# Optimization experiments

Hardware: AMD Instinct MI355X
Metric: run time of the kernel (lower is better)

Reference implementation:

```python
import jax, jax.numpy as jnp
import numpy as np

IN_CH, C_M, C_N = 512, 512, 128
B, H, W = 16, 56, 56


def setup_inputs() -> dict:
    key = jax.random.key(0)
    ks = jax.random.split(key, 7)
    s = 1.0 / np.sqrt(IN_CH)
    return {
        "x": jax.random.normal(ks[0], (B, IN_CH, H, W), dtype=jnp.float32),
        "wA": jax.random.uniform(ks[1], (C_M, IN_CH), jnp.float32, -s, s),
        "bA": jax.random.uniform(ks[2], (C_M,), jnp.float32, -s, s),
        "wB": jax.random.uniform(ks[3], (C_N, IN_CH), jnp.float32, -s, s),
        "bB": jax.random.uniform(ks[4], (C_N,), jnp.float32, -s, s),
        "wV": jax.random.uniform(ks[5], (C_N, IN_CH), jnp.float32, -s, s),
        "bV": jax.random.uniform(ks[6], (C_N,), jnp.float32, -s, s),
        "K": 1,
    }


def reference(x, wA, bA, wB, bB, wV, bV, K):
    b, c, h, w = x.shape
    c_m, c_n = wA.shape[0], wB.shape[0]
    batch = b // K
    hw = h * w
    N = K * hw
    # 1x1 convs == channel-wise matmuls
    A = jnp.einsum('bchw,mc->bmhw', x, wA) + bA[None, :, None, None]
    Bf = jnp.einsum('bchw,nc->bnhw', x, wB) + bB[None, :, None, None]
    Vf = jnp.einsum('bchw,nc->bnhw', x, wV) + bV[None, :, None, None]
    # (batch, c_m, K*h*w)
    tmpA = A.reshape(batch, K, c_m, hw).transpose(0, 2, 1, 3).reshape(batch, c_m, N)
    # softmax over the spatial dim N (torch Softmax() on 2D -> dim=1)
    tmpB = Bf.reshape(batch, K, c_n, hw).transpose(0, 2, 1, 3).reshape(batch, c_n, N)
    attB = jax.nn.softmax(tmpB, axis=-1).transpose(0, 2, 1)  # (batch, N, c_n)
    # softmax over channel dim c_n
    tmpV = Vf.reshape(batch, K, c_n, hw).transpose(0, 1, 3, 2).reshape(batch, N, c_n)
    attV = jax.nn.softmax(tmpV, axis=-1).transpose(0, 2, 1)  # (batch, c_n, N)
    G = jnp.matmul(tmpA, attB)   # (batch, c_m, c_n) global descriptors
    Z = jnp.matmul(G, attV)      # (batch, c_m, N) distribute
    Z = Z.reshape(batch, c_m, K, hw).transpose(0, 2, 1, 3).reshape(b, c_m, h, w)
    return Z
```

## Files before the change

kernel.cpp:

```cpp
#include <hip/hip_runtime.h>
#include <hip/hip_bf16.h>

#define BATCH 16
#define CIN   512
#define HW    3136
#define CM    512
#define CN    128

typedef short short8 __attribute__((ext_vector_type(8)));
typedef float f32x4  __attribute__((ext_vector_type(4)));

#define MFMA(a,b,c) __builtin_amdgcn_mfma_f32_16x16x32_bf16((a),(b),(c),0,0,0)

__device__ __forceinline__ void cvt_store8(__bf16* dst, const float* src) {
  const f32x4 a = *(const f32x4*)src;
  const f32x4 b = *(const f32x4*)(src + 4);
  __attribute__((aligned(16))) __bf16 t[8];
  t[0] = (__bf16)a[0]; t[1] = (__bf16)a[1]; t[2] = (__bf16)a[2]; t[3] = (__bf16)a[3];
  t[4] = (__bf16)b[0]; t[5] = (__bf16)b[1]; t[6] = (__bf16)b[2]; t[7] = (__bf16)b[3];
  *(uint4*)dst = *(uint4*)t;
}

__global__ __launch_bounds__(256) void conv_bv_kernel(
    const float* __restrict__ x,
    const float* __restrict__ wB, const float* __restrict__ wV,
    const float* __restrict__ bB, const float* __restrict__ bV,
    __bf16* __restrict__ BVB, __bf16* __restrict__ attVT,
    float* __restrict__ bsum)
{
  const int s0  = blockIdx.x * 64;
  const int b   = blockIdx.y;
  const int tid = threadIdx.x;
  const int lane = tid & 63, w = tid >> 6;
  const int l15  = lane & 15, q = lane >> 4;

  __shared__ __attribute__((aligned(16))) char smem[46080];
  __bf16* Wt = (__bf16*)smem;
  __bf16* Xt = (__bf16*)(smem + 36864);
  __bf16* T  = (__bf16*)smem;
  __shared__ float Vm[2][64];
  __shared__ float Vs[2][64];

  f32x4 acc[4][4] = {};
  const float* xb = x + (size_t)b*CIN*HW + s0;
  const int colg = tid & 7, row0 = tid >> 3;
  const int cl = 2*(tid >> 3);

  for (int k0 = 0; k0 < CIN; k0 += 64) {
    #pragma unroll
    for (int p = 0; p < 8; ++p) {
      int row = row0 + 32*p;
      const float* src = (row < 128) ? (wB + row*512) : (wV + (row-128)*512);
      cvt_store8(&Wt[row*72 + colg*8], src + k0 + colg*8);
    }
    {
      const float* r0 = xb + (size_t)(k0 + cl)*HW + colg*8;
      const float* r1 = r0 + HW;
      f32x4 a0 = *(const f32x4*)r0, a1 = *(const f32x4*)(r0 + 4);
      f32x4 b0 = *(const f32x4*)r1, b1 = *(const f32x4*)(r1 + 4);
      float va[8] = {a0[0],a0[1],a0[2],a0[3],a1[0],a1[1],a1[2],a1[3]};
      float vb[8] = {b0[0],b0[1],b0[2],b0[3],b1[0],b1[1],b1[2],b1[3]};
      const int off = ((cl >> 3) ^ colg)*8 + (cl & 7);
      #pragma unroll
      for (int j = 0; j < 8; ++j) {
        int s = colg*8 + j;
        __attribute__((aligned(4))) __bf16 pairv[2] = { (__bf16)va[j], (__bf16)vb[j] };
        *(unsigned int*)&Xt[s*72 + off] = *(unsigned int*)pairv;
      }
    }
    __syncthreads();
    #pragma unroll
    for (int kk = 0; kk < 2; ++kk) {
      short8 a[4], bb[4];
      #pragma unroll
      for (int mi = 0; mi < 4; ++mi)
        a[mi] = *(short8*)&Wt[(w*64 + mi*16 + l15)*72 + kk*32 + q*8];
      #pragma unroll
      for (int si = 0; si < 4; ++si) {
        int s = si*16 + l15;
        int oct = (kk*4 + q) ^ (si*2 + (l15 >> 3));
        bb[si] = *(short8*)&Xt[s*72 + oct*8];
      }
      #pragma unroll
      for (int mi = 0; mi < 4; ++mi)
        #pragma unroll
        for (int si = 0; si < 4; ++si)
          acc[mi][si] = MFMA(a[mi], bb[si], acc[mi][si]);
    }
    __syncthreads();
  }

  float bias[4][4];
  #pragma unroll
  for (int mi = 0; mi < 4; ++mi)
    #pragma unroll
    for (int r = 0; r < 4; ++r) {
      int nch = w*64 + mi*16 + q*4 + r;
      bias[mi][r] = (nch < CN) ? bB[nch] : bV[nch - CN];
    }

  if (w < 2) {
    const size_t outb = (size_t)b * CN * HW;
    float psum[4][4] = {};
    #pragma unroll
    for (int mi = 0; mi < 4; ++mi)
      #pragma unroll
      for (int si = 0; si < 4; ++si) {
        int s = s0 + si*16 + l15;
        #pragma unroll
        for (int r = 0; r < 4; ++r) {
          int nch = w*64 + mi*16 + q*4 + r;
          __bf16 bv = (__bf16)(acc[mi][si][r] + bias[mi][r]);
          BVB[outb + (size_t)nch*HW + s] = bv;
          psum[mi][r] += __expf((float)bv);
        }
      }
    #pragma unroll
    for (int mi = 0; mi < 4; ++mi)
      #pragma unroll
      for (int r = 0; r < 4; ++r) {
        float v = psum[mi][r];
        v += __shfl_xor(v, 1); v += __shfl_xor(v, 2);
        v += __shfl_xor(v, 4); v += __shfl_xor(v, 8);
        if (l15 == 0) {
          int nch = w*64 + mi*16 + q*4 + r;
          atomicAdd(&bsum[b*CN + nch], v);
        }
      }
  } else {
    #pragma unroll
    for (int si = 0; si < 4; ++si) {
      float m = -1e30f;
      #pragma unroll
      for (int mi = 0; mi < 4; ++mi)
        #pragma unroll
        for (int r = 0; r < 4; ++r)
          m = fmaxf(m, acc[mi][si][r] + bias[mi][r]);
      m = fmaxf(m, __shfl_xor(m, 16));
      m = fmaxf(m, __shfl_xor(m, 32));
      if (q == 0) Vm[w-2][si*16 + l15] = m;
    }
  }
  __syncthreads();
  if (w >= 2) {
    #pragma unroll
    for (int si = 0; si < 4; ++si) {
      int idx = si*16 + l15;
      float ms = fmaxf(Vm[0][idx], Vm[1][idx]);
      float ssum = 0.f;
      #pragma unroll
      for (int mi = 0; mi < 4; ++mi)
        #pragma unroll
        for (int r = 0; r < 4; ++r) {
          float e = __expf(acc[mi][si][r] + bias[mi][r] - ms);
          acc[mi][si][r] = e;
          ssum += e;
        }
      ssum += __shfl_xor(ssum, 16);
      ssum += __shfl_xor(ssum, 32);
      if (q == 0) Vs[w-2][idx] = ssum;
    }
  }
  __syncthreads();
  if (w >= 2) {
    #pragma unroll
    for (int si = 0; si < 4; ++si) {
      int idx = si*16 + l15;
      float inv = 1.0f / (Vs[0][idx] + Vs[1][idx]);
      #pragma unroll
      for (int mi = 0; mi < 4; ++mi)
        #pragma unroll
        for (int r = 0; r < 4; ++r) {
          int j = (w-2)*64 + mi*16 + q*4 + r;
          T[idx*136 + j] = (__bf16)(acc[mi][si][r] * inv);
        }
    }
  }
  __syncthreads();
  __bf16* dst = attVT + ((size_t)b*HW + s0)*CN;
  #pragma unroll
  for (int k = 0; k < 4; ++k) {
    int chunk = tid + 256*k;
    int row = chunk >> 4, oct = chunk & 15;
    *(uint4*)&dst[(size_t)row*CN + oct*8] = *(uint4*)&T[row*136 + oct*8];
  }
}

__global__ __launch_bounds__(256) void h_gemm_kernel(
    const float* __restrict__ x, const __bf16* __restrict__ BVB,
    const float* __restrict__ bsum, float* __restrict__ H)
{
  const int c0 = blockIdx.x * 128, b = blockIdx.y, kc = blockIdx.z;
  const int tid = threadIdx.x, lane = tid & 63, w = tid >> 6;
  const int l15 = lane & 15, q = lane >> 4;

  __shared__ __attribute__((aligned(16))) __bf16 At[128*72];
  __shared__ __attribute__((aligned(16))) __bf16 Bt[128*72];
  f32x4 acc[8][2] = {};

  const float* xb = x + ((size_t)b*CIN + c0)*HW;
  const __bf16* ab = BVB + (size_t)b*CN*HW;
  const float* bsb = bsum + b*CN;
  const int colg = tid & 7, row0 = tid >> 3;

  float irow[4];
  #pragma unroll
  for (int p = 0; p < 4; ++p) irow[p] = 1.0f / bsb[row0 + 32*p];

  for (int ki = 0; ki < 7; ++ki) {
    int k0 = kc*448 + ki*64;
    #pragma unroll
    for (int p = 0; p < 4; ++p) {
      int row = row0 + 32*p;
      cvt_store8(&At[row*72 + colg*8], xb + (size_t)row*HW + k0 + colg*8);
    }
    #pragma unroll
    for (int p = 0; p < 4; ++p) {
      int row = row0 + 32*p;
      uint4 rawv = *(const uint4*)(ab + (size_t)row*HW + k0 + colg*8);
      const __bf16* v = (const __bf16*)&rawv;
      __attribute__((aligned(16))) __bf16 t[8];
      #pragma unroll
      for (int j = 0; j < 8; ++j)
        t[j] = (__bf16)(__expf((float)v[j]) * irow[p]);
      *(uint4*)&Bt[row*72 + colg*8] = *(uint4*)t;
    }
    __syncthreads();
    #pragma unroll
    for (int kk = 0; kk < 2; ++kk) {
      short8 a[8], bb[2];
      #pragma unroll
      for (int mi = 0; mi < 8; ++mi)
        a[mi] = *(short8*)&At[(mi*16 + l15)*72 + kk*32 + q*8];
      #pragma unroll
      for (int ni = 0; ni < 2; ++ni)
        bb[ni] = *(short8*)&Bt[(w*32 + ni*16 + l15)*72 + kk*32 + q*8];
      #pragma unroll
      for (int mi = 0; mi < 8; ++mi)
        #pragma unroll
        for (int ni = 0; ni < 2; ++ni)
          acc[mi][ni] = MFMA(a[mi], bb[ni], acc[mi][ni]);
    }
    __syncthreads();
  }

  float* Hb = H + (size_t)b*CIN*CN;
  #pragma unroll
  for (int mi = 0; mi < 8; ++mi)
    #pragma unroll
    for (int ni = 0; ni < 2; ++ni)
      #pragma unroll
      for (int r = 0; r < 4; ++r) {
        int c = c0 + mi*16 + q*4 + r;
        int n = w*32 + ni*16 + l15;
        atomicAdd(&Hb[c*CN + n], acc[mi][ni][r]);
      }
}

__global__ __launch_bounds__(256) void g_gemm_kernel(
    const float* __restrict__ wA, const float* __restrict__ bA,
    const float* __restrict__ H, __bf16* __restrict__ G)
{
  const int m0 = blockIdx.x * 64, b = blockIdx.y;
  const int tid = threadIdx.x, lane = tid & 63, w = tid >> 6;
  const int l15 = lane & 15, q = lane >> 4;

  __shared__ __attribute__((aligned(16))) __bf16 At[64*72];
  __shared__ __attribute__((aligned(16))) __bf16 Bt[128*72];
  f32x4 acc[4][2] = {};

  const float* Hb = H + (size_t)b*CIN*CN;
  const int colg = tid & 7, row0 = tid >> 3;
  const int nn = tid & 127, gh = tid >> 7;

  for (int k0 = 0; k0 < CIN; k0 += 64) {
    #pragma unroll
    for (int p = 0; p < 2; ++p) {
      int row = row0 + 32*p;
      cvt_store8(&At[row*72 + colg*8], wA + (size_t)(m0+row)*CIN + k0 + colg*8);
    }
    #pragma unroll
    for (int p = 0; p < 4; ++p) {
      int g = gh + 2*p;
      __attribute__((aligned(16))) __bf16 tmp[8];
      #pragma unroll
      for (int j = 0; j < 8; ++j)
        tmp[j] = (__bf16)Hb[(size_t)(k0 + g*8 + j)*CN + nn];
      *(uint4*)&Bt[nn*72 + g*8] = *(uint4*)tmp;
    }
    __syncthreads();
    #pragma unroll
    for (int kk = 0; kk < 2; ++kk) {
      short8 a[4], bb[2];
      #pragma unroll
      for (int mi = 0; mi < 4; ++mi)
        a[mi] = *(short8*)&At[(mi*16 + l15)*72 + kk*32 + q*8];
      #pragma unroll
      for (int ni = 0; ni < 2; ++ni)
        bb[ni] = *(short8*)&Bt[(w*32 + ni*16 + l15)*72 + kk*32 + q*8];
      #pragma unroll
      for (int mi = 0; mi < 4; ++mi)
        #pragma unroll
        for (int ni = 0; ni < 2; ++ni)
          acc[mi][ni] = MFMA(a[mi], bb[ni], acc[mi][ni]);
    }
    __syncthreads();
  }

  #pragma unroll
  for (int mi = 0; mi < 4; ++mi)
    #pragma unroll
    for (int ni = 0; ni < 2; ++ni)
      #pragma unroll
      for (int r = 0; r < 4; ++r) {
        int m = m0 + mi*16 + q*4 + r;
        int n = w*32 + ni*16 + l15;
        G[((size_t)b*CM + m)*CN + n] = (__bf16)(acc[mi][ni][r] + bA[m]);
      }
}

__global__ __launch_bounds__(256) void z_gemm_kernel(
    const __bf16* __restrict__ G, const __bf16* __restrict__ attVT,
    float* __restrict__ out)
{
  const int m0 = blockIdx.x * 128, s0 = blockIdx.y * 64, b = blockIdx.z;
  const int tid = threadIdx.x, lane = tid & 63, w = tid >> 6;
  const int l15 = lane & 15, q = lane >> 4;

  __shared__ __attribute__((aligned(16))) __bf16 At[128*136];
  __shared__ __attribute__((aligned(16))) __bf16 Bt[64*136];

  const __bf16* Gb = G + ((size_t)b*CM + m0)*CN;
  const __bf16* Vb = attVT + ((size_t)b*HW + s0)*CN;
  const int g = tid & 15, r0 = tid >> 4;
  #pragma unroll
  for (int p = 0; p < 8; ++p) {
    int row = r0 + 16*p;
    *(uint4*)&At[row*136 + g*8] = *(const uint4*)(Gb + (size_t)row*CN + g*8);
  }
  #pragma unroll
  for (int p = 0; p < 4; ++p) {
    int row = r0 + 16*p;
    *(uint4*)&Bt[row*136 + g*8] = *(const uint4*)(Vb + (size_t)row*CN + g*8);
  }
  __syncthreads();

  f32x4 acc[8] = {};
  #pragma unroll
  for (int kk = 0; kk < 4; ++kk) {
    short8 bb = *(short8*)&Bt[(w*16 + l15)*136 + kk*32 + q*8];
    #pragma unroll
    for (int mi = 0; mi < 8; ++mi) {
      short8 a = *(short8*)&At[(mi*16 + l15)*136 + kk*32 + q*8];
      acc[mi] = MFMA(a, bb, acc[mi]);
    }
  }

  const int s = s0 + w*16 + l15;
  #pragma unroll
  for (int mi = 0; mi < 8; ++mi)
    #pragma unroll
    for (int r = 0; r < 4; ++r) {
      int m = m0 + mi*16 + q*4 + r;
      out[((size_t)b*CM + m)*HW + s] = acc[mi][r];
    }
}

extern "C" void kernel_launch(void* const* d_in, const int* in_sizes, int n_in,
                              void* d_out, int out_size, void* d_ws, size_t ws_size,
                              hipStream_t stream)
{
  (void)in_sizes; (void)n_in; (void)out_size; (void)ws_size;
  const float* x  = (const float*)d_in[0];
  const float* wA = (const float*)d_in[1];
  const float* bA = (const float*)d_in[2];
  const float* wB = (const float*)d_in[3];
  const float* bB = (const float*)d_in[4];
  const float* wV = (const float*)d_in[5];
  const float* bV = (const float*)d_in[6];
  float* out = (float*)d_out;

  char* ws = (char*)d_ws;
  const size_t szBVB   = (size_t)BATCH*CN*HW*2;
  const size_t szAttVT = (size_t)BATCH*HW*CN*2;
  const size_t szH     = (size_t)BATCH*CIN*CN*4;
  const size_t szBsum  = (size_t)BATCH*CN*4;

  char* p = ws;
  __bf16* BVB   = (__bf16*)p; p += szBVB;
  __bf16* attVT = (__bf16*)p; p += szAttVT;
  float*  H     = (float*)p;  p += szH;
  float*  bsum  = (float*)p;  p += szBsum;
  __bf16* G     = (__bf16*)p;

  hipMemsetAsync(H, 0, szH + szBsum, stream);
  conv_bv_kernel<<<dim3(49,16),   256, 0, stream>>>(x, wB, wV, bB, bV, BVB, attVT, bsum);
  h_gemm_kernel <<<dim3(4,16,7),  256, 0, stream>>>(x, BVB, bsum, H);
  g_gemm_kernel <<<dim3(8,16),    256, 0, stream>>>(wA, bA, H, G);
  z_gemm_kernel <<<dim3(4,49,16), 256, 0, stream>>>(G, attVT, out);
}
```

Baseline: 298.5 us.

## Prepack weights into MFMA fragment layout, software-pipeline conv and H GEMM loads

Adds a prep kernel that converts wB/wV once into a bf16 image already laid out as per-lane MFMA fragments, so conv_bv loads weight fragments straight into registers instead of converting and staging them through LDS. conv_bv also double-buffers the x tile in LDS with register prefetch of the next slices, and h_gemm prefetches its next k-slice into registers and halves the channel tile to launch twice as many blocks. z_gemm drops LDS staging and reads G and attVT fragments directly from global memory. This adds a kernel launch and some workspace, raises register pressure, and makes z_gemm rely on cache hits for repeated G reads.

```diff
diff --git a/kernel.cpp b/kernel.cpp
--- a/kernel.cpp
+++ b/kernel.cpp
@@ -21,9 +21,33 @@
   *(uint4*)dst = *(uint4*)t;
 }
 
+__device__ __forceinline__ void cvt_store8v(__bf16* dst, f32x4 a, f32x4 b) {
+  __attribute__((aligned(16))) __bf16 t[8];
+  t[0] = (__bf16)a[0]; t[1] = (__bf16)a[1]; t[2] = (__bf16)a[2]; t[3] = (__bf16)a[3];
+  t[4] = (__bf16)b[0]; t[5] = (__bf16)b[1]; t[6] = (__bf16)b[2]; t[7] = (__bf16)b[3];
+  *(uint4*)dst = *(uint4*)t;
+}
+
+__global__ __launch_bounds__(256) void prep_w_kernel(
+    const float* __restrict__ wB, const float* __restrict__ wV,
+    __bf16* __restrict__ Wimg)
+{
+  const int gid  = blockIdx.x * 256 + threadIdx.x;
+  const int lane = gid & 63;
+  const int kk   = (gid >> 6) & 1;
+  const int mi   = (gid >> 7) & 3;
+  const int w    = (gid >> 9) & 3;
+  const int st   = (gid >> 11) & 7;
+  const int row  = w*64 + mi*16 + (lane & 15);
+  const int col  = st*64 + kk*32 + (lane >> 4)*8;
+  const float* src = (row < 128) ? (wB + (size_t)row * CIN)
+                                 : (wV + (size_t)(row - 128) * CIN);
+  cvt_store8(Wimg + (size_t)gid * 8, src + col);
+}
+
 __global__ __launch_bounds__(256) void conv_bv_kernel(
     const float* __restrict__ x,
-    const float* __restrict__ wB, const float* __restrict__ wV,
+    const __bf16* __restrict__ Wimg,
     const float* __restrict__ bB, const float* __restrict__ bV,
     __bf16* __restrict__ BVB, __bf16* __restrict__ attVT,
     float* __restrict__ bsum)
@@ -34,61 +58,87 @@
   const int lane = tid & 63, w = tid >> 6;
   const int l15  = lane & 15, q = lane >> 4;
 
-  __shared__ __attribute__((aligned(16))) char smem[46080];
-  __bf16* Wt = (__bf16*)smem;
-  __bf16* Xt = (__bf16*)(smem + 36864);
-  __bf16* T  = (__bf16*)smem;
+  __shared__ __attribute__((aligned(16))) __bf16 Xt[2][64*72];
+  __bf16* T = (__bf16*)Xt;
   __shared__ float Vm[2][64];
   __shared__ float Vs[2][64];
 
   f32x4 acc[4][4] = {};
   const float* xb = x + (size_t)b*CIN*HW + s0;
-  const int colg = tid & 7, row0 = tid >> 3;
+  const int colg = tid & 7;
   const int cl = 2*(tid >> 3);
-
-  for (int k0 = 0; k0 < CIN; k0 += 64) {
-    #pragma unroll
-    for (int p = 0; p < 8; ++p) {
-      int row = row0 + 32*p;
-      const float* src = (row < 128) ? (wB + row*512) : (wV + (row-128)*512);
-      cvt_store8(&Wt[row*72 + colg*8], src + k0 + colg*8);
-    }
-    {
-      const float* r0 = xb + (size_t)(k0 + cl)*HW + colg*8;
-      const float* r1 = r0 + HW;
-      f32x4 a0 = *(const f32x4*)r0, a1 = *(const f32x4*)(r0 + 4);
-      f32x4 b0 = *(const f32x4*)r1, b1 = *(const f32x4*)(r1 + 4);
-      float va[8] = {a0[0],a0[1],a0[2],a0[3],a1[0],a1[1],a1[2],a1[3]};
-      float vb[8] = {b0[0],b0[1],b0[2],b0[3],b1[0],b1[1],b1[2],b1[3]};
-      const int off = ((cl >> 3) ^ colg)*8 + (cl & 7);
-      #pragma unroll
-      for (int j = 0; j < 8; ++j) {
-        int s = colg*8 + j;
-        __attribute__((aligned(4))) __bf16 pairv[2] = { (__bf16)va[j], (__bf16)vb[j] };
-        *(unsigned int*)&Xt[s*72 + off] = *(unsigned int*)pairv;
-      }
-    }
+  const int xoff = ((cl >> 3) ^ colg)*8 + (cl & 7);
+
+  const char* wbase = (const char*)Wimg + (size_t)w*8192 + (size_t)lane*16;
+
+  short8 wf[8];
+#define WLOAD(ST) do { const char* wp_ = wbase + (ST)*32768; \
+    wf[0]=*(const short8*)(wp_+0);    wf[1]=*(const short8*)(wp_+1024); \
+    wf[2]=*(const short8*)(wp_+2048); wf[3]=*(const short8*)(wp_+3072); \
+    wf[4]=*(const short8*)(wp_+4096); wf[5]=*(const short8*)(wp_+5120); \
+    wf[6]=*(const short8*)(wp_+6144); wf[7]=*(const short8*)(wp_+7168); } while(0)
+
+  f32x4 pf[2][4];
+#define XLOAD(PB, K0) do { \
+    const float* r0_ = xb + (size_t)((K0) + cl)*HW + colg*8; \
+    const float* r1_ = r0_ + HW; \
+    pf[PB][0] = *(const f32x4*)r0_; pf[PB][1] = *(const f32x4*)(r0_ + 4); \
+    pf[PB][2] = *(const f32x4*)r1_; pf[PB][3] = *(const f32x4*)(r1_ + 4); } while(0)
+
+#define XWRITE(BUF, PB) do { \
+    _Pragma("unroll") \
+    for (int j = 0; j < 8; ++j) { \
+      int s_ = colg*8 + j; \
+      union { __bf16 h[2]; unsigned int u; } pv_; \
+      pv_.h[0] = (__bf16)pf[PB][j>>2][j&3]; \
+      pv_.h[1] = (__bf16)pf[PB][2 + (j>>2)][j&3]; \
+      *(unsigned int*)&Xt[BUF][s_*72 + xoff] = pv_.u; \
+    } } while(0)
+
+  XLOAD(0, 0);
+  WLOAD(0);
+  XLOAD(1, 64);
+  XWRITE(0, 0);
+  __syncthreads();
+
+  #pragma unroll
+  for (int st = 0; st < 8; ++st) {
+    const int cur = st & 1;
+    short8 xf0[4];
+    #pragma unroll
+    for (int si = 0; si < 4; ++si) {
+      int s = si*16 + l15;
+      int oct = q ^ (si*2 + (l15 >> 3));
+      xf0[si] = *(short8*)&Xt[cur][s*72 + oct*8];
+    }
+    #pragma unroll
+    for (int mi = 0; mi < 4; ++mi)
+      #pragma unroll
+      for (int si = 0; si < 4; ++si)
+        acc[mi][si] = MFMA(wf[mi*2], xf0[si], acc[mi][si]);
+
+    if (st < 7) XWRITE(cur ^ 1, (st + 1) & 1);
+    if (st < 6) XLOAD(st & 1, (st + 2) * 64);
+
+    short8 xf1[4];
+    #pragma unroll
+    for (int si = 0; si < 4; ++si) {
+      int s = si*16 + l15;
+      int oct = (4 + q) ^ (si*2 + (l15 >> 3));
+      xf1[si] = *(short8*)&Xt[cur][s*72 + oct*8];
+    }
+    #pragma unroll
+    for (int mi = 0; mi < 4; ++mi)
+      #pragma unroll
+      for (int si = 0; si < 4; ++si)
+        acc[mi][si] = MFMA(wf[mi*2+1], xf1[si], acc[mi][si]);
+
+    if (st < 7) WLOAD(st + 1);
     __syncthreads();
-    #pragma unroll
-    for (int kk = 0; kk < 2; ++kk) {
-      short8 a[4], bb[4];
-      #pragma unroll
-      for (int mi = 0; mi < 4; ++mi)
-        a[mi] = *(short8*)&Wt[(w*64 + mi*16 + l15)*72 + kk*32 + q*8];
-      #pragma unroll
-      for (int si = 0; si < 4; ++si) {
-        int s = si*16 + l15;
-        int oct = (kk*4 + q) ^ (si*2 + (l15 >> 3));
-        bb[si] = *(short8*)&Xt[s*72 + oct*8];
-      }
-      #pragma unroll
-      for (int mi = 0; mi < 4; ++mi)
-        #pragma unroll
-        for (int si = 0; si < 4; ++si)
-          acc[mi][si] = MFMA(a[mi], bb[si], acc[mi][si]);
-    }
-    __syncthreads();
-  }
+  }
+#undef WLOAD
+#undef XLOAD
+#undef XWRITE
 
   float bias[4][4];
   #pragma unroll
@@ -190,13 +240,13 @@
     const float* __restrict__ x, const __bf16* __restrict__ BVB,
     const float* __restrict__ bsum, float* __restrict__ H)
 {
-  const int c0 = blockIdx.x * 128, b = blockIdx.y, kc = blockIdx.z;
+  const int c0 = blockIdx.x * 64, b = blockIdx.y, kc = blockIdx.z;
   const int tid = threadIdx.x, lane = tid & 63, w = tid >> 6;
   const int l15 = lane & 15, q = lane >> 4;
 
-  __shared__ __attribute__((aligned(16))) __bf16 At[128*72];
+  __shared__ __attribute__((aligned(16))) __bf16 At[64*72];
   __shared__ __attribute__((aligned(16))) __bf16 Bt[128*72];
-  f32x4 acc[8][2] = {};
+  f32x4 acc[4][2] = {};
 
   const float* xb = x + ((size_t)b*CIN + c0)*HW;
   const __bf16* ab = BVB + (size_t)b*CN*HW;
@@ -207,46 +257,59 @@
   #pragma unroll
   for (int p = 0; p < 4; ++p) irow[p] = 1.0f / bsb[row0 + 32*p];
 
+  f32x4 px[2][2];
+  uint4 pB[4];
+#define HLOAD(K0) do { \
+    _Pragma("unroll") \
+    for (int p = 0; p < 2; ++p) { \
+      const float* s_ = xb + (size_t)(row0 + 32*p)*HW + (K0) + colg*8; \
+      px[p][0] = *(const f32x4*)s_; px[p][1] = *(const f32x4*)(s_ + 4); \
+    } \
+    _Pragma("unroll") \
+    for (int p = 0; p < 4; ++p) \
+      pB[p] = *(const uint4*)(ab + (size_t)(row0 + 32*p)*HW + (K0) + colg*8); \
+  } while(0)
+
+  const int kbase = kc * 448;
+  HLOAD(kbase);
+
   for (int ki = 0; ki < 7; ++ki) {
-    int k0 = kc*448 + ki*64;
+    #pragma unroll
+    for (int p = 0; p < 2; ++p)
+      cvt_store8v(&At[(row0 + 32*p)*72 + colg*8], px[p][0], px[p][1]);
     #pragma unroll
     for (int p = 0; p < 4; ++p) {
-      int row = row0 + 32*p;
-      cvt_store8(&At[row*72 + colg*8], xb + (size_t)row*HW + k0 + colg*8);
-    }
-    #pragma unroll
-    for (int p = 0; p < 4; ++p) {
-      int row = row0 + 32*p;
-      uint4 rawv = *(const uint4*)(ab + (size_t)row*HW + k0 + colg*8);
-      const __bf16* v = (const __bf16*)&rawv;
+      const __bf16* v = (const __bf16*)&pB[p];
       __attribute__((aligned(16))) __bf16 t[8];
       #pragma unroll
       for (int j = 0; j < 8; ++j)
         t[j] = (__bf16)(__expf((float)v[j]) * irow[p]);
-      *(uint4*)&Bt[row*72 + colg*8] = *(uint4*)t;
-    }
+      *(uint4*)&Bt[(row0 + 32*p)*72 + colg*8] = *(uint4*)t;
+    }
+    if (ki < 6) HLOAD(kbase + (ki + 1)*64);
     __syncthreads();
     #pragma unroll
     for (int kk = 0; kk < 2; ++kk) {
-      short8 a[8], bb[2];
-      #pragma unroll
-      for (int mi = 0; mi < 8; ++mi)
+      short8 a[4], bb[2];
+      #pragma unroll
+      for (int mi = 0; mi < 4; ++mi)
         a[mi] = *(short8*)&At[(mi*16 + l15)*72 + kk*32 + q*8];
       #pragma unroll
       for (int ni = 0; ni < 2; ++ni)
         bb[ni] = *(short8*)&Bt[(w*32 + ni*16 + l15)*72 + kk*32 + q*8];
       #pragma unroll
-      for (int mi = 0; mi < 8; ++mi)
+      for (int mi = 0; mi < 4; ++mi)
         #pragma unroll
         for (int ni = 0; ni < 2; ++ni)
           acc[mi][ni] = MFMA(a[mi], bb[ni], acc[mi][ni]);
     }
     __syncthreads();
   }
+#undef HLOAD
 
   float* Hb = H + (size_t)b*CIN*CN;
   #pragma unroll
-  for (int mi = 0; mi < 8; ++mi)
+  for (int mi = 0; mi < 4; ++mi)
     #pragma unroll
     for (int ni = 0; ni < 2; ++ni)
       #pragma unroll
@@ -327,33 +390,25 @@
   const int tid = threadIdx.x, lane = tid & 63, w = tid >> 6;
   const int l15 = lane & 15, q = lane >> 4;
 
-  __shared__ __attribute__((aligned(16))) __bf16 At[128*136];
-  __shared__ __attribute__((aligned(16))) __bf16 Bt[64*136];
-
   const __bf16* Gb = G + ((size_t)b*CM + m0)*CN;
   const __bf16* Vb = attVT + ((size_t)b*HW + s0)*CN;
-  const int g = tid & 15, r0 = tid >> 4;
-  #pragma unroll
-  for (int p = 0; p < 8; ++p) {
-    int row = r0 + 16*p;
-    *(uint4*)&At[row*136 + g*8] = *(const uint4*)(Gb + (size_t)row*CN + g*8);
-  }
-  #pragma unroll
-  for (int p = 0; p < 4; ++p) {
-    int row = r0 + 16*p;
-    *(uint4*)&Bt[row*136 + g*8] = *(const uint4*)(Vb + (size_t)row*CN + g*8);
-  }
-  __syncthreads();
+
+  short8 bb[4];
+  const __bf16* vrow = Vb + (size_t)(w*16 + l15)*CN + q*8;
+  #pragma unroll
+  for (int kk = 0; kk < 4; ++kk)
+    bb[kk] = *(const short8*)(vrow + kk*32);
 
   f32x4 acc[8] = {};
   #pragma unroll
   for (int kk = 0; kk < 4; ++kk) {
-    short8 bb = *(short8*)&Bt[(w*16 + l15)*136 + kk*32 + q*8];
-    #pragma unroll
-    for (int mi = 0; mi < 8; ++mi) {
-      short8 a = *(short8*)&At[(mi*16 + l15)*136 + kk*32 + q*8];
-      acc[mi] = MFMA(a, bb, acc[mi]);
-    }
+    short8 a[8];
+    #pragma unroll
+    for (int mi = 0; mi < 8; ++mi)
+      a[mi] = *(const short8*)(Gb + (size_t)(mi*16 + l15)*CN + kk*32 + q*8);
+    #pragma unroll
+    for (int mi = 0; mi < 8; ++mi)
+      acc[mi] = MFMA(a[mi], bb[kk], acc[mi]);
   }
 
   const int s = s0 + w*16 + l15;
@@ -385,17 +440,20 @@
   const size_t szAttVT = (size_t)BATCH*HW*CN*2;
   const size_t szH     = (size_t)BATCH*CIN*CN*4;
   const size_t szBsum  = (size_t)BATCH*CN*4;
+  const size_t szG     = (size_t)BATCH*CM*CN*2;
 
   char* p = ws;
   __bf16* BVB   = (__bf16*)p; p += szBVB;
   __bf16* attVT = (__bf16*)p; p += szAttVT;
   float*  H     = (float*)p;  p += szH;
   float*  bsum  = (float*)p;  p += szBsum;
-  __bf16* G     = (__bf16*)p;
+  __bf16* G     = (__bf16*)p; p += szG;
+  __bf16* Wimg  = (__bf16*)p;
 
   hipMemsetAsync(H, 0, szH + szBsum, stream);
-  conv_bv_kernel<<<dim3(49,16),   256, 0, stream>>>(x, wB, wV, bB, bV, BVB, attVT, bsum);
-  h_gemm_kernel <<<dim3(4,16,7),  256, 0, stream>>>(x, BVB, bsum, H);
+  prep_w_kernel <<<dim3(64),      256, 0, stream>>>(wB, wV, Wimg);
+  conv_bv_kernel<<<dim3(49,16),   256, 0, stream>>>(x, Wimg, bB, bV, BVB, attVT, bsum);
+  h_gemm_kernel <<<dim3(8,16,7),  256, 0, stream>>>(x, BVB, bsum, H);
   g_gemm_kernel <<<dim3(8,16),    256, 0, stream>>>(wA, bA, H, G);
   z_gemm_kernel <<<dim3(4,49,16), 256, 0, stream>>>(G, attVT, out);
 }
```

New measurement: 323.3 us. +8.3%, slower.
